# Optimization experiments

Hardware: AMD Instinct MI355X
Metric: run time of the kernel (lower is better)

Reference implementation:

```python
import jax, jax.numpy as jnp
import numpy as np

H = 16  # num_heads
D = 1024  # hidden_size

def setup_inputs() -> dict:
    key = jax.random.key(0)
    ks = jax.random.split(key, 9)
    s = 1.0 / np.sqrt(D).astype(np.float32)
    return {
        'x':  jax.random.normal(ks[0], (2, 2048, D), dtype=jnp.float32),
        'wq': jax.random.normal(ks[1], (D, D), dtype=jnp.float32) * s,
        'bq': jax.random.normal(ks[2], (D,), dtype=jnp.float32) * s,
        'wk': jax.random.normal(ks[3], (D, D), dtype=jnp.float32) * s,
        'bk': jax.random.normal(ks[4], (D,), dtype=jnp.float32) * s,
        'wv': jax.random.normal(ks[5], (D, D), dtype=jnp.float32) * s,
        'bv': jax.random.normal(ks[6], (D,), dtype=jnp.float32) * s,
        'wo': jax.random.normal(ks[7], (D, D), dtype=jnp.float32) * s,
        'bo': jax.random.normal(ks[8], (D,), dtype=jnp.float32) * s,
    }

def _split_heads(t):
    # [b, s, (h d)] -> [b, h, s, d]
    b, s, _ = t.shape
    return t.reshape(b, s, H, D // H).transpose(0, 2, 1, 3)

def reference(x, wq, bq, wk, bk, wv, bv, wo, bo):
    q = _split_heads(x @ wq + bq)  # [b, h, s, d]
    k = _split_heads(x @ wk + bk)
    v = _split_heads(x @ wv + bv)
    scale = 1.0 / jnp.sqrt(jnp.asarray(q.shape[-1], q.dtype))
    attn = jnp.einsum('bhqd,bhkd->bhqk', q, k) * scale
    attn = jax.nn.softmax(attn, axis=-1)
    o = jnp.einsum('bhqk,bhkd->bhqd', attn, v)
    b, h, s, d = o.shape
    o = o.transpose(0, 2, 1, 3).reshape(b, s, h * d)  # concat heads
    return o @ wo + bo
```

## Files before the change

### kernel.cpp

```cpp
#include <hip/hip_runtime.h>
#include <stdint.h>
#include <stddef.h>


typedef __bf16 bf16_t;
typedef __bf16 bf16x8 __attribute__((ext_vector_type(8)));
typedef __bf16 bf16x4 __attribute__((ext_vector_type(4)));
typedef __bf16 bf16x2 __attribute__((ext_vector_type(2)));
typedef float  f32x4  __attribute__((ext_vector_type(4)));
typedef float  f32x16 __attribute__((ext_vector_type(16)));
typedef uint32_t u32x4 __attribute__((ext_vector_type(4)));

static constexpr float kQScale = 0.18033688011112042f;

__device__ __forceinline__ void gload_lds16(const bf16_t* g, bf16_t* l) {
  __builtin_amdgcn_global_load_lds((__attribute__((address_space(1))) void*)(void*)g,
                                   (__attribute__((address_space(3))) void*)l, 16, 0, 0);
}

__device__ __forceinline__ uint32_t pk_bf16(float lo, float hi) {
  bf16x2 v; v[0] = (bf16_t)lo; v[1] = (bf16_t)hi;
  return __builtin_bit_cast(uint32_t, v);
}

__global__ __launch_bounds__(256) void cast_x_k(const float* __restrict__ x, bf16_t* __restrict__ xb) {
  int i = blockIdx.x * 256 + threadIdx.x;
  float4 v = ((const float4*)x)[i];
  bf16x4 o;
  o[0] = (bf16_t)v.x; o[1] = (bf16_t)v.y; o[2] = (bf16_t)v.z; o[3] = (bf16_t)v.w;
  ((bf16x4*)xb)[i] = o;
}

__global__ __launch_bounds__(256) void transpose_w_k(
    const float* __restrict__ wq, const float* __restrict__ wk,
    const float* __restrict__ wv, const float* __restrict__ wo,
    bf16_t* __restrict__ wqkvT, bf16_t* __restrict__ woT) {
  __shared__ float t[64][65];
  int z = blockIdx.z;
  const float* src = z == 0 ? wq : z == 1 ? wk : z == 2 ? wv : wo;
  bf16_t* dst = z < 3 ? wqkvT + (size_t)z * 1024 * 1024 : woT;
  int n0 = blockIdx.x * 64, k0 = blockIdx.y * 64;
  int c = threadIdx.x & 63, r4 = threadIdx.x >> 6;
#pragma unroll
  for (int i = 0; i < 16; ++i) {
    int r = r4 + i * 4;
    t[r][c] = src[(size_t)(k0 + r) * 1024 + (n0 + c)];
  }
  __syncthreads();
#pragma unroll
  for (int i = 0; i < 16; ++i) {
    int r = r4 + i * 4;
    dst[(size_t)(n0 + r) * 1024 + (k0 + c)] = (bf16_t)t[c][r];
  }
}

template <int EPI>
__global__ __launch_bounds__(256) void gemm_k(
    const bf16_t* __restrict__ A, const bf16_t* __restrict__ Bw,
    bf16_t* __restrict__ Qb, bf16_t* __restrict__ Kb, bf16_t* __restrict__ Vb,
    const float* __restrict__ bq, const float* __restrict__ bk, const float* __restrict__ bv,
    float* __restrict__ outF, const float* __restrict__ bo) {
  __shared__ alignas(16) bf16_t As[128 * 32];
  __shared__ alignas(16) bf16_t Bs[128 * 32];
  const int tid = threadIdx.x;
  const int lane = tid & 63;
  const int w = tid >> 6, wr = w >> 1, wc = w & 1;
  const int brow = blockIdx.y * 128, bcol = blockIdx.x * 128;
  const int l15 = lane & 15, ko = (lane >> 4) * 8;

  f32x4 acc[4][4] = {};
  const bf16_t* Ab = A + (size_t)brow * 1024;
  const bf16_t* Bb = Bw + (size_t)bcol * 1024;

  const int e0 = tid * 8;
  const int r0 = e0 >> 5, c0 = e0 & 31;

  for (int k0 = 0; k0 < 1024; k0 += 32) {
    gload_lds16(Ab + (size_t)r0 * 1024 + k0 + c0, &As[e0]);
    gload_lds16(Ab + (size_t)(r0 + 64) * 1024 + k0 + c0, &As[e0 + 2048]);
    gload_lds16(Bb + (size_t)r0 * 1024 + k0 + c0, &Bs[e0]);
    gload_lds16(Bb + (size_t)(r0 + 64) * 1024 + k0 + c0, &Bs[e0 + 2048]);
    __syncthreads();
    bf16x8 af[4], bfg[4];
#pragma unroll
    for (int i = 0; i < 4; ++i)
      af[i] = *(const bf16x8*)&As[(wr * 64 + i * 16 + l15) * 32 + ko];
#pragma unroll
    for (int i = 0; i < 4; ++i)
      bfg[i] = *(const bf16x8*)&Bs[(wc * 64 + i * 16 + l15) * 32 + ko];
#pragma unroll
    for (int i = 0; i < 4; ++i)
#pragma unroll
      for (int j = 0; j < 4; ++j)
        acc[i][j] = __builtin_amdgcn_mfma_f32_16x16x32_bf16(af[i], bfg[j], acc[i][j], 0, 0, 0);
    __syncthreads();
  }

#pragma unroll
  for (int i = 0; i < 4; ++i) {
    const int gm0 = brow + wr * 64 + i * 16 + ((lane >> 4) << 2);
#pragma unroll
    for (int j = 0; j < 4; ++j) {
      const int gn = bcol + wc * 64 + j * 16 + l15;
      if constexpr (EPI == 0) {
        const int mat = gn >> 10;
        const int col = gn & 1023;
        bf16_t* dst = mat == 0 ? Qb : (mat == 1 ? Kb : Vb);
        const float* bias = mat == 0 ? bq : (mat == 1 ? bk : bv);
        const float scl = mat == 0 ? kQScale : 1.0f;
        const float bsv = bias[col];
        const int h = col >> 6, dd = col & 63;
#pragma unroll
        for (int r = 0; r < 4; ++r) {
          const int m = gm0 + r;
          const int b = m >> 11, s = m & 2047;
          dst[((((size_t)b * 16 + h) * 2048 + s) * 64 + dd)] = (bf16_t)((acc[i][j][r] + bsv) * scl);
        }
      } else {
        const float bsv = bo[gn];
#pragma unroll
        for (int r = 0; r < 4; ++r)
          outF[(size_t)(gm0 + r) * 1024 + gn] = acc[i][j][r] + bsv;
      }
    }
  }
}

__global__ __launch_bounds__(256) void transpose_v_k(const bf16_t* __restrict__ V, bf16_t* __restrict__ Vt) {
  __shared__ bf16_t t[64][65];
  int bh = blockIdx.y, s0 = blockIdx.x * 64;
  const bf16_t* src = V + (size_t)bh * 2048 * 64;
  bf16_t* dst = Vt + (size_t)bh * 64 * 2048;
  int c = threadIdx.x & 63, r4 = threadIdx.x >> 6;
#pragma unroll
  for (int i = 0; i < 16; ++i) {
    int r = r4 + i * 4;
    t[r][c] = src[(size_t)(s0 + r) * 64 + c];
  }
  __syncthreads();
#pragma unroll
  for (int i = 0; i < 16; ++i) {
    int d = r4 + i * 4;
    dst[(size_t)d * 2048 + s0 + c] = t[c][d];
  }
}

__global__ __launch_bounds__(256, 2) void attn_k(
    const bf16_t* __restrict__ Qb, const bf16_t* __restrict__ Kb,
    const bf16_t* __restrict__ Vt, bf16_t* __restrict__ O) {
  __shared__ alignas(16) bf16_t Ksm[2][4096];
  __shared__ alignas(16) bf16_t Vsm[2][4096];
  const int tid = threadIdx.x, lane = tid & 63, w = tid >> 6;
  const int l31 = lane & 31, hi = lane >> 5;
  const int work = (blockIdx.x & 7) * 64 + (blockIdx.x >> 3);
  const int bh = work >> 4;
  const int q0 = (work & 15) * 128 + w * 32;

  const bf16_t* Qp = Qb + ((size_t)bh * 2048 + q0) * 64;

  const int chunk0 = w * 64 + lane;
  const int srow = chunk0 >> 3;
  const int swzc = (chunk0 & 7) ^ (srow & 7);
  const char* srcK0 = (const char*)(Kb + (size_t)bh * 2048 * 64) + srow * 128 + swzc * 16;
  const char* srcK1 = srcK0 + 32 * 128;
  const char* srcV0 = (const char*)(Vt + (size_t)bh * 64 * 2048) + srow * 4096 + swzc * 16;
  const char* srcV1 = srcV0 + 32 * 4096;

  auto stage = [&](int buf) {
    bf16_t* kb = &Ksm[buf][w * 512];
    bf16_t* vb = &Vsm[buf][w * 512];
    gload_lds16((const bf16_t*)srcK0, kb);
    gload_lds16((const bf16_t*)srcK1, kb + 2048);
    gload_lds16((const bf16_t*)srcV0, vb);
    gload_lds16((const bf16_t*)srcV1, vb + 2048);
    srcK0 += 8192; srcK1 += 8192;
    srcV0 += 128;  srcV1 += 128;
  };

  const int xorv = l31 & 7;
  const bf16_t* kcb[4];
  const bf16_t* vcb[4];
#pragma unroll
  for (int j = 0; j < 4; ++j) {
    const int co = ((j * 2 + hi) ^ xorv) * 8;
    kcb[j] = &Ksm[0][l31 * 64 + co];
    vcb[j] = &Vsm[0][l31 * 64 + co];
  }

  bf16x8 qf[4];
#pragma unroll
  for (int ds = 0; ds < 4; ++ds)
    qf[ds] = *(const bf16x8*)&Qp[(size_t)l31 * 64 + ds * 16 + hi * 8];

  f32x16 o0 = {}, o1 = {};
  float mx = -1e30f, li = 0.0f;

  auto tile_body = [&](int buf) {
    const int bo = buf * 4096;
    bf16x8 kf0[4], kf1[4];
#pragma unroll
    for (int ds = 0; ds < 4; ++ds) {
      kf0[ds] = *(const bf16x8*)(kcb[ds] + bo);
      kf1[ds] = *(const bf16x8*)(kcb[ds] + bo + 2048);
    }
    f32x16 s0 = {}, s1 = {};
    __builtin_amdgcn_s_setprio(1);
#pragma unroll
    for (int ds = 0; ds < 4; ++ds)
      s0 = __builtin_amdgcn_mfma_f32_32x32x16_bf16(kf0[ds], qf[ds], s0, 0, 0, 0);
#pragma unroll
    for (int ds = 0; ds < 4; ++ds)
      s1 = __builtin_amdgcn_mfma_f32_32x32x16_bf16(kf1[ds], qf[ds], s1, 0, 0, 0);
    __builtin_amdgcn_s_setprio(0);
    bf16x8 vf0[4], vf1[4];
#pragma unroll
    for (int ks = 0; ks < 4; ++ks) {
      vf0[ks] = *(const bf16x8*)(vcb[ks] + bo);
      vf1[ks] = *(const bf16x8*)(vcb[ks] + bo + 2048);
    }

    float m8[8];
#pragma unroll
    for (int r = 0; r < 8; ++r)
      m8[r] = fmaxf(fmaxf(s0[r], s0[r + 8]), fmaxf(s1[r], s1[r + 8]));
    float m4a = fmaxf(m8[0], m8[4]), m4b = fmaxf(m8[1], m8[5]);
    float m4c = fmaxf(m8[2], m8[6]), m4d = fmaxf(m8[3], m8[7]);
    float tmax = fmaxf(fmaxf(m4a, m4b), fmaxf(m4c, m4d));
    tmax = fmaxf(tmax, __shfl_xor(tmax, 32));

    if (__any(tmax > mx + 8.0f)) {
      const float mn = fmaxf(mx, tmax);
      const float corr = __builtin_amdgcn_exp2f(mx - mn);
      mx = mn;
      li *= corr;
#pragma unroll
      for (int r = 0; r < 16; ++r) { o0[r] *= corr; o1[r] *= corr; }
    }

    float ra = 0.f, rb = 0.f, rc = 0.f, rd = 0.f;
#pragma unroll
    for (int r = 0; r < 4; ++r) {
      float p0 = __builtin_amdgcn_exp2f(s0[r] - mx);       s0[r] = p0; ra += p0;
      float p1 = __builtin_amdgcn_exp2f(s0[r + 4] - mx);   s0[r + 4] = p1; rb += p1;
      float p2 = __builtin_amdgcn_exp2f(s0[r + 8] - mx);   s0[r + 8] = p2; rc += p2;
      float p3 = __builtin_amdgcn_exp2f(s0[r + 12] - mx);  s0[r + 12] = p3; rd += p3;
      float p4 = __builtin_amdgcn_exp2f(s1[r] - mx);       s1[r] = p4; ra += p4;
      float p5 = __builtin_amdgcn_exp2f(s1[r + 4] - mx);   s1[r + 4] = p5; rb += p5;
      float p6 = __builtin_amdgcn_exp2f(s1[r + 8] - mx);   s1[r + 8] = p6; rc += p6;
      float p7 = __builtin_amdgcn_exp2f(s1[r + 12] - mx);  s1[r + 12] = p7; rd += p7;
    }
    float rs = (ra + rb) + (rc + rd);
    rs += __shfl_xor(rs, 32);
    li += rs;

    uint32_t pw0[8], pw1[8];
#pragma unroll
    for (int g = 0; g < 4; ++g) {
      pw0[g * 2 + 0] = pk_bf16(s0[4 * g + 0], s0[4 * g + 1]);
      pw0[g * 2 + 1] = pk_bf16(s0[4 * g + 2], s0[4 * g + 3]);
      pw1[g * 2 + 0] = pk_bf16(s1[4 * g + 0], s1[4 * g + 1]);
      pw1[g * 2 + 1] = pk_bf16(s1[4 * g + 2], s1[4 * g + 3]);
    }

#pragma unroll
    for (int st = 0; st < 2; ++st) {
      uint32_t (&pw)[8] = st ? pw1 : pw0;
#pragma unroll
      for (int ks = 0; ks < 2; ++ks) {
        const uint32_t A0 = pw[(2 * ks) * 2 + 0], A1 = pw[(2 * ks) * 2 + 1];
        const uint32_t B0 = pw[(2 * ks + 1) * 2 + 0], B1 = pw[(2 * ks + 1) * 2 + 1];
        const uint32_t Z0 = hi ? A0 : B0;
        const uint32_t Z1 = hi ? A1 : B1;
        const uint32_t sZ0 = (uint32_t)__shfl_xor((int)Z0, 32);
        const uint32_t sZ1 = (uint32_t)__shfl_xor((int)Z1, 32);
        u32x4 fw;
        fw[0] = hi ? sZ0 : A0;
        fw[1] = hi ? sZ1 : A1;
        fw[2] = hi ? B0 : sZ0;
        fw[3] = hi ? B1 : sZ1;
        const bf16x8 pf = __builtin_bit_cast(bf16x8, fw);
        __builtin_amdgcn_s_setprio(1);
        o0 = __builtin_amdgcn_mfma_f32_32x32x16_bf16(vf0[st * 2 + ks], pf, o0, 0, 0, 0);
        o1 = __builtin_amdgcn_mfma_f32_32x32x16_bf16(vf1[st * 2 + ks], pf, o1, 0, 0, 0);
        __builtin_amdgcn_s_setprio(0);
      }
    }
  };

  stage(0);
  __syncthreads();
#pragma unroll 1
  for (int t = 0; t < 32; t += 2) {
    stage(1);
    tile_body(0);
    __syncthreads();
    if (t + 2 < 32) stage(0);
    tile_body(1);
    if (t + 2 < 32) __syncthreads();
  }

  const int b = bh >> 4, h = bh & 15;
  const float inv = 1.0f / li;
  const size_t row = (size_t)b * 2048 + q0 + l31;
#pragma unroll
  for (int g = 0; g < 4; ++g) {
    bf16x4 p0, p1;
#pragma unroll
    for (int r = 0; r < 4; ++r) {
      p0[r] = (bf16_t)(o0[4 * g + r] * inv);
      p1[r] = (bf16_t)(o1[4 * g + r] * inv);
    }
    *(bf16x4*)&O[row * 1024 + h * 64 + 0  + g * 8 + hi * 4] = p0;
    *(bf16x4*)&O[row * 1024 + h * 64 + 32 + g * 8 + hi * 4] = p1;
  }
}

extern "C" void kernel_launch(void* const* d_in, const int* in_sizes, int n_in,
                              void* d_out, int out_size, void* d_ws, size_t ws_size,
                              hipStream_t stream) {
  const float* x  = (const float*)d_in[0];
  const float* wq = (const float*)d_in[1];
  const float* bq = (const float*)d_in[2];
  const float* wk = (const float*)d_in[3];
  const float* bk = (const float*)d_in[4];
  const float* wv = (const float*)d_in[5];
  const float* bv = (const float*)d_in[6];
  const float* wo = (const float*)d_in[7];
  const float* bo = (const float*)d_in[8];
  float* out = (float*)d_out;

  if (ws_size < ((size_t)48 << 20)) return;
  char* ws = (char*)d_ws;
  bf16_t* xb  = (bf16_t*)(ws);
  bf16_t* wT  = (bf16_t*)(ws + ((size_t)8 << 20));
  bf16_t* woT = wT + (size_t)3072 * 1024;
  bf16_t* Qb  = (bf16_t*)(ws + ((size_t)16 << 20));
  bf16_t* Kb  = (bf16_t*)(ws + ((size_t)24 << 20));
  bf16_t* Vb  = (bf16_t*)(ws + ((size_t)32 << 20));
  bf16_t* Vt  = (bf16_t*)(ws + ((size_t)40 << 20));
  bf16_t* O   = xb;

  cast_x_k<<<4096, 256, 0, stream>>>(x, xb);
  transpose_w_k<<<dim3(16, 16, 4), 256, 0, stream>>>(wq, wk, wv, wo, wT, woT);
  gemm_k<0><<<dim3(24, 32), 256, 0, stream>>>(xb, wT, Qb, Kb, Vb, bq, bk, bv, nullptr, nullptr);
  transpose_v_k<<<dim3(32, 32), 256, 0, stream>>>(Vb, Vt);
  attn_k<<<512, 256, 0, stream>>>(Qb, Kb, Vt, O);
  gemm_k<1><<<dim3(8, 32), 256, 0, stream>>>(O, woT, nullptr, nullptr, nullptr,
                                             nullptr, nullptr, nullptr, out, bo);
}
```

Measured before the change: 132.7 us.

## Fuse prep kernels, write V transposed from QKV GEMM, retile output GEMM

Merges the x cast and weight transpose into one prep launch. The QKV GEMM epilogue now writes V directly in transposed [b,h,d,s] layout with packed 4-element stores, which removes the separate V transpose kernel and its round trip through memory. The output projection gets its own kernel with 128x64 tiles, doubling the block count to 512 to fill more CUs. Together these cut two launches and some global traffic, at the cost of an unbalanced prep grid and fewer MFMAs per block in the output GEMM.

```diff
diff --git a/kernel.cpp b/kernel.cpp
--- a/kernel.cpp
+++ b/kernel.cpp
@@ -23,20 +23,25 @@
   return __builtin_bit_cast(uint32_t, v);
 }
 
-__global__ __launch_bounds__(256) void cast_x_k(const float* __restrict__ x, bf16_t* __restrict__ xb) {
-  int i = blockIdx.x * 256 + threadIdx.x;
-  float4 v = ((const float4*)x)[i];
-  bf16x4 o;
-  o[0] = (bf16_t)v.x; o[1] = (bf16_t)v.y; o[2] = (bf16_t)v.z; o[3] = (bf16_t)v.w;
-  ((bf16x4*)xb)[i] = o;
-}
-
-__global__ __launch_bounds__(256) void transpose_w_k(
+__global__ __launch_bounds__(256) void prep_k(
+    const float* __restrict__ x, bf16_t* __restrict__ xb,
     const float* __restrict__ wq, const float* __restrict__ wk,
     const float* __restrict__ wv, const float* __restrict__ wo,
     bf16_t* __restrict__ wqkvT, bf16_t* __restrict__ woT) {
   __shared__ float t[64][65];
-  int z = blockIdx.z;
+  const int z = blockIdx.z;
+  if (z == 4) {
+    const int blk = blockIdx.y * 16 + blockIdx.x;
+#pragma unroll
+    for (int c = 0; c < 16; ++c) {
+      const int i = c * 65536 + blk * 256 + threadIdx.x;
+      float4 v = ((const float4*)x)[i];
+      bf16x4 o;
+      o[0] = (bf16_t)v.x; o[1] = (bf16_t)v.y; o[2] = (bf16_t)v.z; o[3] = (bf16_t)v.w;
+      ((bf16x4*)xb)[i] = o;
+    }
+    return;
+  }
   const float* src = z == 0 ? wq : z == 1 ? wk : z == 2 ? wv : wo;
   bf16_t* dst = z < 3 ? wqkvT + (size_t)z * 1024 * 1024 : woT;
   int n0 = blockIdx.x * 64, k0 = blockIdx.y * 64;
@@ -54,12 +59,10 @@
   }
 }
 
-template <int EPI>
-__global__ __launch_bounds__(256) void gemm_k(
+__global__ __launch_bounds__(256) void gemm_qkv_k(
     const bf16_t* __restrict__ A, const bf16_t* __restrict__ Bw,
-    bf16_t* __restrict__ Qb, bf16_t* __restrict__ Kb, bf16_t* __restrict__ Vb,
-    const float* __restrict__ bq, const float* __restrict__ bk, const float* __restrict__ bv,
-    float* __restrict__ outF, const float* __restrict__ bo) {
+    bf16_t* __restrict__ Qb, bf16_t* __restrict__ Kb, bf16_t* __restrict__ Vt,
+    const float* __restrict__ bq, const float* __restrict__ bk, const float* __restrict__ bv) {
   __shared__ alignas(16) bf16_t As[128 * 32];
   __shared__ alignas(16) bf16_t Bs[128 * 32];
   const int tid = threadIdx.x;
@@ -96,52 +99,83 @@
     __syncthreads();
   }
 
+  const int mat = bcol >> 10;
 #pragma unroll
   for (int i = 0; i < 4; ++i) {
     const int gm0 = brow + wr * 64 + i * 16 + ((lane >> 4) << 2);
+    const int b = gm0 >> 11, s0 = gm0 & 2047;
 #pragma unroll
     for (int j = 0; j < 4; ++j) {
       const int gn = bcol + wc * 64 + j * 16 + l15;
-      if constexpr (EPI == 0) {
-        const int mat = gn >> 10;
-        const int col = gn & 1023;
-        bf16_t* dst = mat == 0 ? Qb : (mat == 1 ? Kb : Vb);
-        const float* bias = mat == 0 ? bq : (mat == 1 ? bk : bv);
+      const int col = gn & 1023;
+      const int h = col >> 6, dd = col & 63;
+      if (mat == 2) {
+        const float bsv = bv[col];
+        bf16x4 pk;
+#pragma unroll
+        for (int r = 0; r < 4; ++r) pk[r] = (bf16_t)(acc[i][j][r] + bsv);
+        *(bf16x4*)&Vt[(((size_t)b * 16 + h) * 64 + dd) * 2048 + s0] = pk;
+      } else {
+        bf16_t* dst = mat == 0 ? Qb : Kb;
+        const float bsv = (mat == 0 ? bq : bk)[col];
         const float scl = mat == 0 ? kQScale : 1.0f;
-        const float bsv = bias[col];
-        const int h = col >> 6, dd = col & 63;
-#pragma unroll
-        for (int r = 0; r < 4; ++r) {
-          const int m = gm0 + r;
-          const int b = m >> 11, s = m & 2047;
-          dst[((((size_t)b * 16 + h) * 2048 + s) * 64 + dd)] = (bf16_t)((acc[i][j][r] + bsv) * scl);
-        }
-      } else {
-        const float bsv = bo[gn];
 #pragma unroll
         for (int r = 0; r < 4; ++r)
-          outF[(size_t)(gm0 + r) * 1024 + gn] = acc[i][j][r] + bsv;
+          dst[((((size_t)b * 16 + h) * 2048 + (s0 + r)) * 64 + dd)] = (bf16_t)((acc[i][j][r] + bsv) * scl);
       }
     }
   }
 }
 
-__global__ __launch_bounds__(256) void transpose_v_k(const bf16_t* __restrict__ V, bf16_t* __restrict__ Vt) {
-  __shared__ bf16_t t[64][65];
-  int bh = blockIdx.y, s0 = blockIdx.x * 64;
-  const bf16_t* src = V + (size_t)bh * 2048 * 64;
-  bf16_t* dst = Vt + (size_t)bh * 64 * 2048;
-  int c = threadIdx.x & 63, r4 = threadIdx.x >> 6;
-#pragma unroll
-  for (int i = 0; i < 16; ++i) {
-    int r = r4 + i * 4;
-    t[r][c] = src[(size_t)(s0 + r) * 64 + c];
-  }
-  __syncthreads();
-#pragma unroll
-  for (int i = 0; i < 16; ++i) {
-    int d = r4 + i * 4;
-    dst[(size_t)d * 2048 + s0 + c] = t[c][d];
+__global__ __launch_bounds__(256) void gemm_out_k(
+    const bf16_t* __restrict__ A, const bf16_t* __restrict__ Bw,
+    float* __restrict__ outF, const float* __restrict__ bo) {
+  __shared__ alignas(16) bf16_t As[128 * 32];
+  __shared__ alignas(16) bf16_t Bs[64 * 32];
+  const int tid = threadIdx.x;
+  const int lane = tid & 63;
+  const int w = tid >> 6;
+  const int brow = blockIdx.y * 128, bcol = blockIdx.x * 64;
+  const int l15 = lane & 15, ko = (lane >> 4) * 8;
+
+  f32x4 acc[2][4] = {};
+  const bf16_t* Ab = A + (size_t)brow * 1024;
+  const bf16_t* Bb = Bw + (size_t)bcol * 1024;
+
+  const int e0 = tid * 8;
+  const int r0 = e0 >> 5, c0 = e0 & 31;
+
+  for (int k0 = 0; k0 < 1024; k0 += 32) {
+    gload_lds16(Ab + (size_t)r0 * 1024 + k0 + c0, &As[e0]);
+    gload_lds16(Ab + (size_t)(r0 + 64) * 1024 + k0 + c0, &As[e0 + 2048]);
+    gload_lds16(Bb + (size_t)r0 * 1024 + k0 + c0, &Bs[e0]);
+    __syncthreads();
+    bf16x8 af[2], bfg[4];
+#pragma unroll
+    for (int i = 0; i < 2; ++i)
+      af[i] = *(const bf16x8*)&As[(w * 32 + i * 16 + l15) * 32 + ko];
+#pragma unroll
+    for (int j = 0; j < 4; ++j)
+      bfg[j] = *(const bf16x8*)&Bs[(j * 16 + l15) * 32 + ko];
+#pragma unroll
+    for (int i = 0; i < 2; ++i)
+#pragma unroll
+      for (int j = 0; j < 4; ++j)
+        acc[i][j] = __builtin_amdgcn_mfma_f32_16x16x32_bf16(af[i], bfg[j], acc[i][j], 0, 0, 0);
+    __syncthreads();
+  }
+
+#pragma unroll
+  for (int i = 0; i < 2; ++i) {
+    const int gm0 = brow + w * 32 + i * 16 + ((lane >> 4) << 2);
+#pragma unroll
+    for (int j = 0; j < 4; ++j) {
+      const int gn = bcol + j * 16 + l15;
+      const float bsv = bo[gn];
+#pragma unroll
+      for (int r = 0; r < 4; ++r)
+        outF[(size_t)(gm0 + r) * 1024 + gn] = acc[i][j][r] + bsv;
+    }
   }
 }
 
@@ -336,15 +370,11 @@
   bf16_t* woT = wT + (size_t)3072 * 1024;
   bf16_t* Qb  = (bf16_t*)(ws + ((size_t)16 << 20));
   bf16_t* Kb  = (bf16_t*)(ws + ((size_t)24 << 20));
-  bf16_t* Vb  = (bf16_t*)(ws + ((size_t)32 << 20));
-  bf16_t* Vt  = (bf16_t*)(ws + ((size_t)40 << 20));
+  bf16_t* Vt  = (bf16_t*)(ws + ((size_t)32 << 20));
   bf16_t* O   = xb;
 
-  cast_x_k<<<4096, 256, 0, stream>>>(x, xb);
-  transpose_w_k<<<dim3(16, 16, 4), 256, 0, stream>>>(wq, wk, wv, wo, wT, woT);
-  gemm_k<0><<<dim3(24, 32), 256, 0, stream>>>(xb, wT, Qb, Kb, Vb, bq, bk, bv, nullptr, nullptr);
-  transpose_v_k<<<dim3(32, 32), 256, 0, stream>>>(Vb, Vt);
+  prep_k<<<dim3(16, 16, 5), 256, 0, stream>>>(x, xb, wq, wk, wv, wo, wT, woT);
+  gemm_qkv_k<<<dim3(24, 32), 256, 0, stream>>>(xb, wT, Qb, Kb, Vt, bq, bk, bv);
   attn_k<<<512, 256, 0, stream>>>(Qb, Kb, Vt, O);
-  gemm_k<1><<<dim3(8, 32), 256, 0, stream>>>(O, woT, nullptr, nullptr, nullptr,
-                                             nullptr, nullptr, nullptr, out, bo);
-}
+  gemm_out_k<<<dim3(16, 32), 256, 0, stream>>>(O, woT, out, bo);
+}
```

Result: faster. 122.7 us (-7.6%).
